# Optimization experiments

Hardware: AMD Instinct MI355X
Metric: run time of the kernel (lower is better)

Reference implementation:

```python
import jax, jax.numpy as jnp
import numpy as np

B = 16384
QD = 2048   # query_dim
KD = 1024   # key_dim
HID = 1024  # hidden_dim = min(QD, KD)
NH = 16     # num_heads
HD = HID // NH  # head_dim = 64
LN_EPS = 1e-5


def _ln(x, w, b):
    m = jnp.mean(x, axis=-1, keepdims=True)
    v = jnp.mean((x - m) ** 2, axis=-1, keepdims=True)
    return (x - m) * jax.lax.rsqrt(v + LN_EPS) * w + b


def _lin(x, W, b):
    return x @ W.T + b


def setup_inputs() -> dict:
    key = jax.random.key(0)
    ks = jax.random.split(key, 12)
    p = lambda k, shape: jax.random.normal(k, shape, jnp.float32) * 0.02
    return dict(
        query_features=jax.random.normal(ks[0], (B, QD), jnp.float32),
        key_features=jax.random.normal(ks[1], (B, KD), jnp.float32),
        Wq=p(ks[2], (HID, QD)), bq=jnp.zeros((HID,), jnp.float32),
        ln_q_w=jnp.ones((HID,), jnp.float32), ln_q_b=jnp.zeros((HID,), jnp.float32),
        Wk=p(ks[3], (HID, KD)), bk=jnp.zeros((HID,), jnp.float32),
        ln_k_w=jnp.ones((HID,), jnp.float32), ln_k_b=jnp.zeros((HID,), jnp.float32),
        Wvq=p(ks[4], (HID, QD)), bvq=jnp.zeros((HID,), jnp.float32),
        Wvk=p(ks[5], (HID, KD)), bvk=jnp.zeros((HID,), jnp.float32),
        Wo=p(ks[6], (QD, HID)), bo=jnp.zeros((QD,), jnp.float32),
        ln_o_w=jnp.ones((QD,), jnp.float32), ln_o_b=jnp.zeros((QD,), jnp.float32),
        Wg1=p(ks[7], (HID, QD + KD)), bg1=jnp.zeros((HID,), jnp.float32),
        Wg2=p(ks[8], (1, HID)), bg2=jnp.zeros((1,), jnp.float32),
        Wc1=p(ks[9], (HID, QD + KD)), bc1=jnp.zeros((HID,), jnp.float32),
        Wc2=p(ks[10], (1, HID)), bc2=jnp.zeros((1,), jnp.float32),
    )


def reference(query_features, key_features,
              Wq, bq, ln_q_w, ln_q_b,
              Wk, bk, ln_k_w, ln_k_b,
              Wvq, bvq, Wvk, bvk,
              Wo, bo, ln_o_w, ln_o_b,
              Wg1, bg1, Wg2, bg2,
              Wc1, bc1, Wc2, bc2):
    b = query_features.shape[0]
    q = _ln(_lin(query_features, Wq, bq), ln_q_w, ln_q_b)      # [B, HID]
    k = _ln(_lin(key_features, Wk, bk), ln_k_w, ln_k_b)        # [B, HID]
    v_q = _lin(query_features, Wvq, bvq)  # computed in torch but unused
    v_k = _lin(key_features, Wvk, bvk)    # [B, HID]
    q = q.reshape(b, NH, HD)
    k = k.reshape(b, NH, HD)
    v_k = v_k.reshape(b, NH, HD)
    # NOTE: attention mixes over the HEAD axis (j == num_heads), per original einsum
    scores = jnp.einsum('bhd,bjd->bhj', q, k) / np.sqrt(HD).astype(np.float32)
    attn = jax.nn.softmax(scores, axis=-1)  # dropout p effectively 0 / eval mode
    attended = jnp.einsum('bhj,bjd->bhd', attn, v_k).reshape(b, HID)
    output = _ln(_lin(attended, Wo, bo), ln_o_w, ln_o_b)       # [B, QD]
    combined = jnp.concatenate([query_features, key_features], axis=1)  # [B, QD+KD]
    gate = jax.nn.sigmoid(_lin(jax.nn.gelu(_lin(combined, Wg1, bg1), approximate=False), Wg2, bg2))
    chem = jax.nn.sigmoid(_lin(jax.nn.gelu(_lin(combined, Wc1, bc1), approximate=False), Wc2, bc2))
    effective_gate = gate * chem  # [B, 1]
    return query_features + effective_gate * output
```

## Files before the change

kernel.cpp:

```cpp
#include <hip/hip_runtime.h>
#include <stdint.h>

#define QD 2048
#define KD 1024
#define HID 1024
#define NH 16
#define HD 64
#define CMBD 3072

typedef float  f32x4   __attribute__((ext_vector_type(4)));
typedef short  short8  __attribute__((ext_vector_type(8)));
typedef short  short4v __attribute__((ext_vector_type(4)));
typedef float  float4v __attribute__((ext_vector_type(4)));

__device__ inline float bf2f(short s) {
  unsigned u = ((unsigned)(unsigned short)s) << 16;
  return __builtin_bit_cast(float, u);
}
__device__ inline short f2bf(float f) {
  unsigned u = __builtin_bit_cast(unsigned, f);
  u = u + 0x7fff + ((u >> 16) & 1);
  return (short)(u >> 16);
}

__global__ void cvt_bf16(const float* __restrict__ s, short* __restrict__ d) {
  size_t i = ((size_t)blockIdx.x * blockDim.x + threadIdx.x) * 4;
  float4v v = *(const float4v*)(s + i);
  short4v o;
  o[0] = f2bf(v[0]); o[1] = f2bf(v[1]); o[2] = f2bf(v[2]); o[3] = f2bf(v[3]);
  *(short4v*)(d + i) = o;
}

__global__ void cvt_concat(const float* __restrict__ s, short* __restrict__ d,
                           int ncols4, int ldd) {
  int i = blockIdx.x * blockDim.x + threadIdx.x;
  int row = i / ncols4;
  int c4  = i - row * ncols4;
  float4v v = *(const float4v*)(s + (size_t)row * (ncols4 * 4) + c4 * 4);
  short4v o;
  o[0] = f2bf(v[0]); o[1] = f2bf(v[1]); o[2] = f2bf(v[2]); o[3] = f2bf(v[3]);
  *(short4v*)(d + (size_t)row * ldd + c4 * 4) = o;
}

#define EPI_NONE 0
#define EPI_GELU 1

typedef const __attribute__((address_space(1))) void gvoid_t;
typedef __attribute__((address_space(3))) void lvoid_t;

#define WAIT_VM(n)  asm volatile("s_waitcnt vmcnt(" #n ")" ::: "memory")

#define APAN(b, kp) (((b) * 2 + (kp)) * 8192)
#define BPAN(b, kp) (32768 + ((b) * 2 + (kp)) * 8192)

#define PHASE_MID                                        \
  __builtin_amdgcn_s_barrier();                          \
  asm volatile("s_waitcnt lgkmcnt(0)" ::: "memory");     \
  __builtin_amdgcn_s_setprio(1);

#define PHASE_END                                        \
  __builtin_amdgcn_s_setprio(0);                         \
  __builtin_amdgcn_s_barrier();

template<int EPI>
__global__ __launch_bounds__(512, 2)
void gemm256(const short* __restrict__ A, size_t lda,
             const short* __restrict__ W,
             const float* __restrict__ bias,
             short* __restrict__ C, int N, int K) {
  extern __shared__ short ls[];
  const int tid  = threadIdx.x;
  const int lane = tid & 63;
  const int wave = tid >> 6;
  const int wm = wave >> 2, wn = wave & 3;
  const int fr = lane & 15, kq4 = lane >> 4;

  const int nwg = gridDim.x * gridDim.y;
  const int lin = blockIdx.y * gridDim.x + blockIdx.x;
  const int cpx = nwg >> 3;
  const int nid = (lin & 7) * cpx + (lin >> 3);
  const int bx = nid % gridDim.x, by = nid / gridDim.x;
  const size_t rowBase = (size_t)by * 256;
  const size_t colBase = (size_t)bx * 256;

  const int NTT = K >> 6;

  f32x4 acc[8][4];
#pragma unroll
  for (int mi = 0; mi < 8; mi++)
#pragma unroll
    for (int ni = 0; ni < 4; ni++) acc[mi][ni] = (f32x4){0.f, 0.f, 0.f, 0.f};

  const int frsw = (kq4 ^ ((fr >> 1) & 3)) * 8;

  const int grow  = tid >> 2;
  const int slotx = (tid & 3) ^ ((tid >> 3) & 3);
  const short* gAlo = A + (rowBase + grow) * lda + slotx * 8;
  const short* gAhi = gAlo + (size_t)128 * lda;
  const short* gBlo = W + (colBase + grow) * (size_t)K + slotx * 8;
  const short* gBhi = gBlo + (size_t)128 * K;
  short* const sdst = ls + tid * 8;

  auto STG_A = [&](int panOff, int kcol) {
    __builtin_amdgcn_global_load_lds((gvoid_t*)(gAlo + kcol), (lvoid_t*)(sdst + panOff),        16, 0, 0);
    __builtin_amdgcn_global_load_lds((gvoid_t*)(gAhi + kcol), (lvoid_t*)(sdst + panOff + 4096), 16, 0, 0);
  };
  auto STG_B = [&](int panOff, int kcol) {
    __builtin_amdgcn_global_load_lds((gvoid_t*)(gBlo + kcol), (lvoid_t*)(sdst + panOff),        16, 0, 0);
    __builtin_amdgcn_global_load_lds((gvoid_t*)(gBhi + kcol), (lvoid_t*)(sdst + panOff + 4096), 16, 0, 0);
  };

  STG_A(APAN(0, 0), 0);  STG_A(APAN(0, 1), 32);
  STG_B(BPAN(0, 0), 0);  STG_B(BPAN(0, 1), 32);
  STG_B(BPAN(1, 0), 64); STG_B(BPAN(1, 1), 96);
  WAIT_VM(4);
  __builtin_amdgcn_s_barrier();

  short8 fa0[8], fa1[8], fb0[4], fb1[4];

  for (int t = 0; t < NTT; t += 2) {
    const bool more = (t + 2 < NTT);
    const int kA1 = (t + 1) * 64;
    const int kE2 = (t + 2) * 64;
    const int kO3 = (t + 3) * 64;

#pragma unroll
    for (int m = 0; m < 4; m++) {
      const int r = (wm * 128 + m * 16 + fr) * 32 + frsw;
      fa0[m * 2 + 0] = *(const short8*)(ls + APAN(0, 0) + r);
      fa0[m * 2 + 1] = *(const short8*)(ls + APAN(0, 1) + r);
    }
#pragma unroll
    for (int n = 0; n < 2; n++) {
      const int r = (wn * 64 + n * 16 + fr) * 32 + frsw;
      fb0[n * 2 + 0] = *(const short8*)(ls + BPAN(0, 0) + r);
      fb0[n * 2 + 1] = *(const short8*)(ls + BPAN(0, 1) + r);
    }
    STG_A(APAN(1, 0), kA1);
    PHASE_MID
#pragma unroll
    for (int m = 0; m < 4; m++)
#pragma unroll
      for (int n = 0; n < 2; n++) {
        acc[m][n] = __builtin_amdgcn_mfma_f32_16x16x32_bf16(fa0[m*2+0], fb0[n*2+0], acc[m][n], 0, 0, 0);
        acc[m][n] = __builtin_amdgcn_mfma_f32_16x16x32_bf16(fa0[m*2+1], fb0[n*2+1], acc[m][n], 0, 0, 0);
      }
    PHASE_END

#pragma unroll
    for (int n = 0; n < 2; n++) {
      const int r = (wn * 64 + (n + 2) * 16 + fr) * 32 + frsw;
      fb1[n * 2 + 0] = *(const short8*)(ls + BPAN(0, 0) + r);
      fb1[n * 2 + 1] = *(const short8*)(ls + BPAN(0, 1) + r);
    }
    STG_A(APAN(1, 1), kA1 + 32);
    PHASE_MID
#pragma unroll
    for (int m = 0; m < 4; m++)
#pragma unroll
      for (int n = 0; n < 2; n++) {
        acc[m][n+2] = __builtin_amdgcn_mfma_f32_16x16x32_bf16(fa0[m*2+0], fb1[n*2+0], acc[m][n+2], 0, 0, 0);
        acc[m][n+2] = __builtin_amdgcn_mfma_f32_16x16x32_bf16(fa0[m*2+1], fb1[n*2+1], acc[m][n+2], 0, 0, 0);
      }
    PHASE_END

#pragma unroll
    for (int m = 0; m < 4; m++) {
      const int r = (wm * 128 + (m + 4) * 16 + fr) * 32 + frsw;
      fa1[m * 2 + 0] = *(const short8*)(ls + APAN(0, 0) + r);
      fa1[m * 2 + 1] = *(const short8*)(ls + APAN(0, 1) + r);
    }
    if (more) STG_B(BPAN(0, 0), kE2);
    PHASE_MID
#pragma unroll
    for (int m = 0; m < 4; m++)
#pragma unroll
      for (int n = 0; n < 2; n++) {
        acc[m+4][n] = __builtin_amdgcn_mfma_f32_16x16x32_bf16(fa1[m*2+0], fb0[n*2+0], acc[m+4][n], 0, 0, 0);
        acc[m+4][n] = __builtin_amdgcn_mfma_f32_16x16x32_bf16(fa1[m*2+1], fb0[n*2+1], acc[m+4][n], 0, 0, 0);
      }
    PHASE_END

    if (more) STG_B(BPAN(0, 1), kE2 + 32);
    PHASE_MID
#pragma unroll
    for (int m = 0; m < 4; m++)
#pragma unroll
      for (int n = 0; n < 2; n++) {
        acc[m+4][n+2] = __builtin_amdgcn_mfma_f32_16x16x32_bf16(fa1[m*2+0], fb1[n*2+0], acc[m+4][n+2], 0, 0, 0);
        acc[m+4][n+2] = __builtin_amdgcn_mfma_f32_16x16x32_bf16(fa1[m*2+1], fb1[n*2+1], acc[m+4][n+2], 0, 0, 0);
      }
    __builtin_amdgcn_s_setprio(0);
    if (more) { WAIT_VM(4); } else { WAIT_VM(0); }
    __builtin_amdgcn_s_barrier();

#pragma unroll
    for (int m = 0; m < 4; m++) {
      const int r = (wm * 128 + m * 16 + fr) * 32 + frsw;
      fa0[m * 2 + 0] = *(const short8*)(ls + APAN(1, 0) + r);
      fa0[m * 2 + 1] = *(const short8*)(ls + APAN(1, 1) + r);
    }
#pragma unroll
    for (int n = 0; n < 2; n++) {
      const int r = (wn * 64 + n * 16 + fr) * 32 + frsw;
      fb0[n * 2 + 0] = *(const short8*)(ls + BPAN(1, 0) + r);
      fb0[n * 2 + 1] = *(const short8*)(ls + BPAN(1, 1) + r);
    }
    if (more) STG_A(APAN(0, 0), kE2);
    PHASE_MID
#pragma unroll
    for (int m = 0; m < 4; m++)
#pragma unroll
      for (int n = 0; n < 2; n++) {
        acc[m][n] = __builtin_amdgcn_mfma_f32_16x16x32_bf16(fa0[m*2+0], fb0[n*2+0], acc[m][n], 0, 0, 0);
        acc[m][n] = __builtin_amdgcn_mfma_f32_16x16x32_bf16(fa0[m*2+1], fb0[n*2+1], acc[m][n], 0, 0, 0);
      }
    PHASE_END

#pragma unroll
    for (int n = 0; n < 2; n++) {
      const int r = (wn * 64 + (n + 2) * 16 + fr) * 32 + frsw;
      fb1[n * 2 + 0] = *(const short8*)(ls + BPAN(1, 0) + r);
      fb1[n * 2 + 1] = *(const short8*)(ls + BPAN(1, 1) + r);
    }
    if (more) STG_A(APAN(0, 1), kE2 + 32);
    PHASE_MID
#pragma unroll
    for (int m = 0; m < 4; m++)
#pragma unroll
      for (int n = 0; n < 2; n++) {
        acc[m][n+2] = __builtin_amdgcn_mfma_f32_16x16x32_bf16(fa0[m*2+0], fb1[n*2+0], acc[m][n+2], 0, 0, 0);
        acc[m][n+2] = __builtin_amdgcn_mfma_f32_16x16x32_bf16(fa0[m*2+1], fb1[n*2+1], acc[m][n+2], 0, 0, 0);
      }
    PHASE_END

#pragma unroll
    for (int m = 0; m < 4; m++) {
      const int r = (wm * 128 + (m + 4) * 16 + fr) * 32 + frsw;
      fa1[m * 2 + 0] = *(const short8*)(ls + APAN(1, 0) + r);
      fa1[m * 2 + 1] = *(const short8*)(ls + APAN(1, 1) + r);
    }
    if (more) STG_B(BPAN(1, 0), kO3);
    PHASE_MID
#pragma unroll
    for (int m = 0; m < 4; m++)
#pragma unroll
      for (int n = 0; n < 2; n++) {
        acc[m+4][n] = __builtin_amdgcn_mfma_f32_16x16x32_bf16(fa1[m*2+0], fb0[n*2+0], acc[m+4][n], 0, 0, 0);
        acc[m+4][n] = __builtin_amdgcn_mfma_f32_16x16x32_bf16(fa1[m*2+1], fb0[n*2+1], acc[m+4][n], 0, 0, 0);
      }
    PHASE_END

    if (more) STG_B(BPAN(1, 1), kO3 + 32);
    PHASE_MID
#pragma unroll
    for (int m = 0; m < 4; m++)
#pragma unroll
      for (int n = 0; n < 2; n++) {
        acc[m+4][n+2] = __builtin_amdgcn_mfma_f32_16x16x32_bf16(fa1[m*2+0], fb1[n*2+0], acc[m+4][n+2], 0, 0, 0);
        acc[m+4][n+2] = __builtin_amdgcn_mfma_f32_16x16x32_bf16(fa1[m*2+1], fb1[n*2+1], acc[m+4][n+2], 0, 0, 0);
      }
    __builtin_amdgcn_s_setprio(0);
    if (more) { WAIT_VM(4); }
    __builtin_amdgcn_s_barrier();
  }

#pragma unroll
  for (int mi = 0; mi < 8; mi++) {
    const size_t row0 = rowBase + wm * 128 + mi * 16 + kq4 * 4;
#pragma unroll
    for (int ni = 0; ni < 4; ni++) {
      const int col = (int)colBase + wn * 64 + ni * 16 + fr;
      const float bv = bias[col];
#pragma unroll
      for (int j = 0; j < 4; j++) {
        float x = acc[mi][ni][j] + bv;
        if (EPI == EPI_GELU) x = 0.5f * x * (1.f + erff(x * 0.70710678118f));
        C[(row0 + j) * (size_t)N + col] = f2bf(x);
      }
    }
  }
}

__device__ inline float2 block_sum2(float a, float b, float* sc) {
#pragma unroll
  for (int o = 32; o >= 1; o >>= 1) {
    a += __shfl_down(a, o);
    b += __shfl_down(b, o);
  }
  const int lane = threadIdx.x & 63, w = threadIdx.x >> 6;
  const int nw = blockDim.x >> 6;
  if (lane == 0) { sc[w * 2] = a; sc[w * 2 + 1] = b; }
  __syncthreads();
  float ra = 0.f, rb = 0.f;
  for (int i = 0; i < nw; i++) { ra += sc[i * 2]; rb += sc[i * 2 + 1]; }
  __syncthreads();
  return make_float2(ra, rb);
}

__global__ __launch_bounds__(256)
void attn_ln(const short* __restrict__ qp, const short* __restrict__ kv,
             const float* __restrict__ lnqw, const float* __restrict__ lnqb,
             const float* __restrict__ lnkw, const float* __restrict__ lnkb,
             short* __restrict__ att) {
  __shared__ float qs[HID];
  __shared__ float ks[NH * 65];
  __shared__ float vs[HID];
  __shared__ float aw[256];
  __shared__ float red[8];
  const int t = threadIdx.x;
  const size_t row = blockIdx.x;

  short4v q4 = *(const short4v*)(qp + row * HID + t * 4);
  short4v k4 = *(const short4v*)(kv + row * 2048 + t * 4);
  short4v v4 = *(const short4v*)(kv + row * 2048 + 1024 + t * 4);
  float qv[4], kvv[4];
  float sq = 0.f, sqq = 0.f, sk = 0.f, skk = 0.f;
#pragma unroll
  for (int i = 0; i < 4; i++) {
    qv[i] = bf2f(q4[i]); sq += qv[i]; sqq += qv[i] * qv[i];
    kvv[i] = bf2f(k4[i]); sk += kvv[i]; skk += kvv[i] * kvv[i];
  }
  float2 rq = block_sum2(sq, sqq, red);
  float mq = rq.x / HID, vq = rq.y / HID - mq * mq;
  float rsq = rsqrtf(vq + 1e-5f);
  float2 rk = block_sum2(sk, skk, red);
  float mk = rk.x / HID, vv = rk.y / HID - mk * mk;
  float rsk = rsqrtf(vv + 1e-5f);
#pragma unroll
  for (int i = 0; i < 4; i++) {
    const int idx = t * 4 + i;
    qs[idx] = (qv[i] - mq) * rsq * lnqw[idx] + lnqb[idx];
    ks[(idx >> 6) * 65 + (idx & 63)] = (kvv[i] - mk) * rsk * lnkw[idx] + lnkb[idx];
    vs[idx] = bf2f(v4[i]);
  }
  __syncthreads();

  const int h = t >> 4, j = t & 15;
  float s = 0.f;
#pragma unroll 8
  for (int d = 0; d < 64; d++) s += qs[h * 64 + d] * ks[j * 65 + d];
  s *= 0.125f;
  float mx = s;
#pragma unroll
  for (int o = 8; o >= 1; o >>= 1) mx = fmaxf(mx, __shfl_xor(mx, o, 16));
  float e = __expf(s - mx);
  float sum = e;
#pragma unroll
  for (int o = 8; o >= 1; o >>= 1) sum += __shfl_xor(sum, o, 16);
  aw[t] = e / sum;
  __syncthreads();

  const int dB = (t & 15) * 4;
  float o0 = 0.f, o1 = 0.f, o2 = 0.f, o3 = 0.f;
#pragma unroll
  for (int jj = 0; jj < 16; jj++) {
    const float w = aw[h * 16 + jj];
    const float* vp = &vs[jj * 64 + dB];
    o0 += w * vp[0]; o1 += w * vp[1]; o2 += w * vp[2]; o3 += w * vp[3];
  }
  short4v o4;
  o4[0] = f2bf(o0); o4[1] = f2bf(o1); o4[2] = f2bf(o2); o4[3] = f2bf(o3);
  *(short4v*)(att + row * HID + h * 64 + dB) = o4;
}

__global__ __launch_bounds__(256)
void gate_kernel(const short* __restrict__ hgc,
                 const float* __restrict__ wg2, const float* __restrict__ bg2,
                 const float* __restrict__ wc2, const float* __restrict__ bc2,
                 float* __restrict__ eg) {
  __shared__ float red[8];
  const int t = threadIdx.x;
  const size_t row = blockIdx.x;
  short4v g4 = *(const short4v*)(hgc + row * 2048 + t * 4);
  short4v c4 = *(const short4v*)(hgc + row * 2048 + 1024 + t * 4);
  float sg = 0.f, sc = 0.f;
#pragma unroll
  for (int i = 0; i < 4; i++) {
    sg += bf2f(g4[i]) * wg2[t * 4 + i];
    sc += bf2f(c4[i]) * wc2[t * 4 + i];
  }
  float2 r = block_sum2(sg, sc, red);
  if (t == 0) {
    float g = 1.f / (1.f + __expf(-(r.x + bg2[0])));
    float c = 1.f / (1.f + __expf(-(r.y + bc2[0])));
    eg[row] = g * c;
  }
}

__global__ __launch_bounds__(256)
void final_kernel(const short* __restrict__ opre, const float* __restrict__ qf,
                  const float* __restrict__ eg,
                  const float* __restrict__ lnow, const float* __restrict__ lnob,
                  float* __restrict__ out) {
  __shared__ float red[8];
  const int t = threadIdx.x;
  const size_t row = blockIdx.x;
  short8 o8 = *(const short8*)(opre + row * QD + t * 8);
  float x[8];
  float s = 0.f, ss = 0.f;
#pragma unroll
  for (int i = 0; i < 8; i++) { x[i] = bf2f(o8[i]); s += x[i]; ss += x[i] * x[i]; }
  float2 r = block_sum2(s, ss, red);
  float m = r.x / QD, v = r.y / QD - m * m;
  float rs = rsqrtf(v + 1e-5f);
  float g = eg[row];
  float4v oa, ob;
#pragma unroll
  for (int i = 0; i < 8; i++) {
    const int c = t * 8 + i;
    float y = (x[i] - m) * rs * lnow[c] + lnob[c];
    float r2 = qf[row * QD + c] + g * y;
    if (i < 4) oa[i] = r2; else ob[i - 4] = r2;
  }
  *(float4v*)(out + row * QD + t * 8) = oa;
  *(float4v*)(out + row * QD + t * 8 + 4) = ob;
}

extern "C" void kernel_launch(void* const* d_in, const int* in_sizes, int n_in,
                              void* d_out, int out_size, void* d_ws, size_t ws_size,
                              hipStream_t stream) {
  const float* qf   = (const float*)d_in[0];
  const float* kf   = (const float*)d_in[1];
  const float* Wq   = (const float*)d_in[2];
  const float* bq   = (const float*)d_in[3];
  const float* lnqw = (const float*)d_in[4];
  const float* lnqb = (const float*)d_in[5];
  const float* Wk   = (const float*)d_in[6];
  const float* bk   = (const float*)d_in[7];
  const float* lnkw = (const float*)d_in[8];
  const float* lnkb = (const float*)d_in[9];
  const float* Wvk  = (const float*)d_in[12];
  const float* bvk  = (const float*)d_in[13];
  const float* Wo   = (const float*)d_in[14];
  const float* bo   = (const float*)d_in[15];
  const float* lnow = (const float*)d_in[16];
  const float* lnob = (const float*)d_in[17];
  const float* Wg1  = (const float*)d_in[18];
  const float* bg1  = (const float*)d_in[19];
  const float* Wg2  = (const float*)d_in[20];
  const float* bg2  = (const float*)d_in[21];
  const float* Wc1  = (const float*)d_in[22];
  const float* bc1  = (const float*)d_in[23];
  const float* Wc2  = (const float*)d_in[24];
  const float* bc2  = (const float*)d_in[25];

  const int rows = in_sizes[0] / QD;

  char* ws = (char*)d_ws;
  size_t off = 0;
  auto alloc = [&](size_t bytes) -> char* {
    char* p = ws + off;
    off += (bytes + 255) & ~(size_t)255;
    return p;
  };
  short* cmb  = (short*)alloc((size_t)rows * CMBD * 2);
  short* wqb  = (short*)alloc((size_t)HID * QD * 2);
  short* wkv  = (short*)alloc((size_t)2 * HID * KD * 2);
  short* wob  = (short*)alloc((size_t)QD * HID * 2);
  short* wgc  = (short*)alloc((size_t)2 * HID * CMBD * 2);
  short* hgc  = (short*)alloc((size_t)rows * 2048 * 2);
  short* qp   = (short*)alloc((size_t)rows * HID * 2);
  short* kvp  = (short*)alloc((size_t)rows * 2048 * 2);
  float* eg   = (float*)alloc((size_t)rows * 4);
  float* bgc  = (float*)alloc(2048 * 4);
  float* bkv  = (float*)alloc(2048 * 4);
  short* att  = hgc;
  short* opre = cmb;

  hipMemcpyAsync(bgc, bg1, HID * 4, hipMemcpyDeviceToDevice, stream);
  hipMemcpyAsync(bgc + HID, bc1, HID * 4, hipMemcpyDeviceToDevice, stream);
  hipMemcpyAsync(bkv, bk, HID * 4, hipMemcpyDeviceToDevice, stream);
  hipMemcpyAsync(bkv + HID, bvk, HID * 4, hipMemcpyDeviceToDevice, stream);

  cvt_concat<<<rows * 2, 256, 0, stream>>>(qf, cmb, QD / 4, CMBD);
  cvt_concat<<<rows, 256, 0, stream>>>(kf, cmb + QD, KD / 4, CMBD);
  cvt_bf16<<<(HID * QD / 4) / 256, 256, 0, stream>>>(Wq, wqb);
  cvt_bf16<<<(HID * KD / 4) / 256, 256, 0, stream>>>(Wk, wkv);
  cvt_bf16<<<(HID * KD / 4) / 256, 256, 0, stream>>>(Wvk, wkv + (size_t)HID * KD);
  cvt_bf16<<<(QD * HID / 4) / 256, 256, 0, stream>>>(Wo, wob);
  cvt_bf16<<<(HID * CMBD / 4) / 256, 256, 0, stream>>>(Wg1, wgc);
  cvt_bf16<<<(HID * CMBD / 4) / 256, 256, 0, stream>>>(Wc1, wgc + (size_t)HID * CMBD);

  hipFuncSetAttribute((const void*)gemm256<EPI_GELU>,
                      hipFuncAttributeMaxDynamicSharedMemorySize, 131072);
  hipFuncSetAttribute((const void*)gemm256<EPI_NONE>,
                      hipFuncAttributeMaxDynamicSharedMemorySize, 131072);

  const dim3 blk(512);
  const int mt = rows / 256;
  const size_t lds = 131072;

  gemm256<EPI_GELU><<<dim3(2048 / 256, mt), blk, lds, stream>>>(cmb, CMBD, wgc, bgc, hgc, 2048, CMBD);
  gate_kernel<<<rows, 256, 0, stream>>>(hgc, Wg2, bg2, Wc2, bc2, eg);
  gemm256<EPI_NONE><<<dim3(1024 / 256, mt), blk, lds, stream>>>(cmb, CMBD, wqb, bq, qp, 1024, QD);
  gemm256<EPI_NONE><<<dim3(2048 / 256, mt), blk, lds, stream>>>(cmb + QD, CMBD, wkv, bkv, kvp, 2048, KD);
  attn_ln<<<rows, 256, 0, stream>>>(qp, kvp, lnqw, lnqb, lnkw, lnkb, att);
  gemm256<EPI_NONE><<<dim3(2048 / 256, mt), blk, lds, stream>>>(att, HID, wob, bo, opre, 2048, HID);
  final_kernel<<<rows, 256, 0, stream>>>(opre, qf, eg, lnow, lnob, (float*)d_out);
}
```

Baseline: 634.4 us.

## Fuse gate/chem second-layer dot products into GEMM epilogue via atomics

The gate GEMM epilogue now applies GELU and immediately dots each row with the second-layer weights. It reduces across lanes and atomically accumulates per-row partial sums into a zeroed buffer, so the bf16 hidden activations are never written and the separate gate kernel is removed. The final kernel applies the sigmoids and combines gate and chem. Separately, the attention LayerNorm merges its two block reductions into one. The cost is float atomics, which add contention and make summation order nondeterministic, plus an extra memset.

```diff
diff --git a/kernel.cpp b/kernel.cpp
--- a/kernel.cpp
+++ b/kernel.cpp
@@ -44,6 +44,7 @@
 
 #define EPI_NONE 0
 #define EPI_GELU 1
+#define EPI_GATE 2
 
 typedef const __attribute__((address_space(1))) void gvoid_t;
 typedef __attribute__((address_space(3))) void lvoid_t;
@@ -67,7 +68,8 @@
 void gemm256(const short* __restrict__ A, size_t lda,
              const short* __restrict__ W,
              const float* __restrict__ bias,
-             short* __restrict__ C, int N, int K) {
+             short* __restrict__ C, int N, int K,
+             const float* __restrict__ w2, float* __restrict__ egp, int rowsTot) {
   extern __shared__ short ls[];
   const int tid  = threadIdx.x;
   const int lane = tid & 63;
@@ -265,35 +267,78 @@
     __builtin_amdgcn_s_barrier();
   }
 
-#pragma unroll
-  for (int mi = 0; mi < 8; mi++) {
-    const size_t row0 = rowBase + wm * 128 + mi * 16 + kq4 * 4;
+  if (EPI == EPI_GATE) {
+    float w2v[4], bvv[4];
 #pragma unroll
     for (int ni = 0; ni < 4; ni++) {
-      const int col = (int)colBase + wn * 64 + ni * 16 + fr;
-      const float bv = bias[col];
+      const int c = (int)colBase + wn * 64 + ni * 16 + fr;
+      w2v[ni] = w2[c]; bvv[ni] = bias[c];
+    }
+    const int half = (colBase >= 1024) ? 1 : 0;
+#pragma unroll
+    for (int mi = 0; mi < 8; mi++) {
+      float sj[4] = {0.f, 0.f, 0.f, 0.f};
+#pragma unroll
+      for (int ni = 0; ni < 4; ni++)
+#pragma unroll
+        for (int j = 0; j < 4; j++) {
+          float x = acc[mi][ni][j] + bvv[ni];
+          float g = 0.5f * x * (1.f + erff(x * 0.70710678118f));
+          sj[j] += g * w2v[ni];
+        }
 #pragma unroll
       for (int j = 0; j < 4; j++) {
-        float x = acc[mi][ni][j] + bv;
-        if (EPI == EPI_GELU) x = 0.5f * x * (1.f + erff(x * 0.70710678118f));
-        C[(row0 + j) * (size_t)N + col] = f2bf(x);
-      }
-    }
-  }
-}
-
-__device__ inline float2 block_sum2(float a, float b, float* sc) {
+#pragma unroll
+        for (int o = 8; o >= 1; o >>= 1) sj[j] += __shfl_xor(sj[j], o);
+        if (fr == 0) {
+          const int row = (int)rowBase + wm * 128 + mi * 16 + kq4 * 4 + j;
+          atomicAdd(egp + half * rowsTot + row, sj[j]);
+        }
+      }
+    }
+  } else {
+#pragma unroll
+    for (int mi = 0; mi < 8; mi++) {
+      const size_t row0 = rowBase + wm * 128 + mi * 16 + kq4 * 4;
+#pragma unroll
+      for (int ni = 0; ni < 4; ni++) {
+        const int col = (int)colBase + wn * 64 + ni * 16 + fr;
+        const float bv = bias[col];
+#pragma unroll
+        for (int j = 0; j < 4; j++) {
+          float x = acc[mi][ni][j] + bv;
+          if (EPI == EPI_GELU) x = 0.5f * x * (1.f + erff(x * 0.70710678118f));
+          C[(row0 + j) * (size_t)N + col] = f2bf(x);
+        }
+      }
+    }
+  }
+}
+
+__device__ inline float4 block_sum4(float a, float b, float c, float d, float* sc) {
 #pragma unroll
   for (int o = 32; o >= 1; o >>= 1) {
-    a += __shfl_down(a, o);
-    b += __shfl_down(b, o);
+    a += __shfl_down(a, o); b += __shfl_down(b, o);
+    c += __shfl_down(c, o); d += __shfl_down(d, o);
   }
   const int lane = threadIdx.x & 63, w = threadIdx.x >> 6;
   const int nw = blockDim.x >> 6;
-  if (lane == 0) { sc[w * 2] = a; sc[w * 2 + 1] = b; }
+  if (lane == 0) { sc[w*4] = a; sc[w*4+1] = b; sc[w*4+2] = c; sc[w*4+3] = d; }
+  __syncthreads();
+  float ra = 0.f, rb = 0.f, rc = 0.f, rd = 0.f;
+  for (int i = 0; i < nw; i++) { ra += sc[i*4]; rb += sc[i*4+1]; rc += sc[i*4+2]; rd += sc[i*4+3]; }
+  __syncthreads();
+  return make_float4(ra, rb, rc, rd);
+}
+__device__ inline float2 block_sum2(float a, float b, float* sc) {
+#pragma unroll
+  for (int o = 32; o >= 1; o >>= 1) { a += __shfl_down(a, o); b += __shfl_down(b, o); }
+  const int lane = threadIdx.x & 63, w = threadIdx.x >> 6;
+  const int nw = blockDim.x >> 6;
+  if (lane == 0) { sc[w*2] = a; sc[w*2+1] = b; }
   __syncthreads();
   float ra = 0.f, rb = 0.f;
-  for (int i = 0; i < nw; i++) { ra += sc[i * 2]; rb += sc[i * 2 + 1]; }
+  for (int i = 0; i < nw; i++) { ra += sc[i*2]; rb += sc[i*2+1]; }
   __syncthreads();
   return make_float2(ra, rb);
 }
@@ -307,7 +352,7 @@
   __shared__ float ks[NH * 65];
   __shared__ float vs[HID];
   __shared__ float aw[256];
-  __shared__ float red[8];
+  __shared__ float red[16];
   const int t = threadIdx.x;
   const size_t row = blockIdx.x;
 
@@ -321,11 +366,10 @@
     qv[i] = bf2f(q4[i]); sq += qv[i]; sqq += qv[i] * qv[i];
     kvv[i] = bf2f(k4[i]); sk += kvv[i]; skk += kvv[i] * kvv[i];
   }
-  float2 rq = block_sum2(sq, sqq, red);
-  float mq = rq.x / HID, vq = rq.y / HID - mq * mq;
+  float4 r4 = block_sum4(sq, sqq, sk, skk, red);
+  float mq = r4.x / HID, vq = r4.y / HID - mq * mq;
   float rsq = rsqrtf(vq + 1e-5f);
-  float2 rk = block_sum2(sk, skk, red);
-  float mk = rk.x / HID, vv = rk.y / HID - mk * mk;
+  float mk = r4.z / HID, vv = r4.w / HID - mk * mk;
   float rsk = rsqrtf(vv + 1e-5f);
 #pragma unroll
   for (int i = 0; i < 4; i++) {
@@ -365,32 +409,9 @@
 }
 
 __global__ __launch_bounds__(256)
-void gate_kernel(const short* __restrict__ hgc,
-                 const float* __restrict__ wg2, const float* __restrict__ bg2,
-                 const float* __restrict__ wc2, const float* __restrict__ bc2,
-                 float* __restrict__ eg) {
-  __shared__ float red[8];
-  const int t = threadIdx.x;
-  const size_t row = blockIdx.x;
-  short4v g4 = *(const short4v*)(hgc + row * 2048 + t * 4);
-  short4v c4 = *(const short4v*)(hgc + row * 2048 + 1024 + t * 4);
-  float sg = 0.f, sc = 0.f;
-#pragma unroll
-  for (int i = 0; i < 4; i++) {
-    sg += bf2f(g4[i]) * wg2[t * 4 + i];
-    sc += bf2f(c4[i]) * wc2[t * 4 + i];
-  }
-  float2 r = block_sum2(sg, sc, red);
-  if (t == 0) {
-    float g = 1.f / (1.f + __expf(-(r.x + bg2[0])));
-    float c = 1.f / (1.f + __expf(-(r.y + bc2[0])));
-    eg[row] = g * c;
-  }
-}
-
-__global__ __launch_bounds__(256)
 void final_kernel(const short* __restrict__ opre, const float* __restrict__ qf,
-                  const float* __restrict__ eg,
+                  const float* __restrict__ egp, int rowsTot,
+                  const float* __restrict__ bg2, const float* __restrict__ bc2,
                   const float* __restrict__ lnow, const float* __restrict__ lnob,
                   float* __restrict__ out) {
   __shared__ float red[8];
@@ -404,7 +425,9 @@
   float2 r = block_sum2(s, ss, red);
   float m = r.x / QD, v = r.y / QD - m * m;
   float rs = rsqrtf(v + 1e-5f);
-  float g = eg[row];
+  float gg = 1.f / (1.f + __expf(-(egp[row] + bg2[0])));
+  float gc = 1.f / (1.f + __expf(-(egp[rowsTot + row] + bc2[0])));
+  float g = gg * gc;
   float4v oa, ob;
 #pragma unroll
   for (int i = 0; i < 8; i++) {
@@ -462,9 +485,10 @@
   short* hgc  = (short*)alloc((size_t)rows * 2048 * 2);
   short* qp   = (short*)alloc((size_t)rows * HID * 2);
   short* kvp  = (short*)alloc((size_t)rows * 2048 * 2);
-  float* eg   = (float*)alloc((size_t)rows * 4);
+  float* egp  = (float*)alloc((size_t)2 * rows * 4);
   float* bgc  = (float*)alloc(2048 * 4);
   float* bkv  = (float*)alloc(2048 * 4);
+  float* w2gc = (float*)alloc(2048 * 4);
   short* att  = hgc;
   short* opre = cmb;
 
@@ -472,6 +496,9 @@
   hipMemcpyAsync(bgc + HID, bc1, HID * 4, hipMemcpyDeviceToDevice, stream);
   hipMemcpyAsync(bkv, bk, HID * 4, hipMemcpyDeviceToDevice, stream);
   hipMemcpyAsync(bkv + HID, bvk, HID * 4, hipMemcpyDeviceToDevice, stream);
+  hipMemcpyAsync(w2gc, Wg2, HID * 4, hipMemcpyDeviceToDevice, stream);
+  hipMemcpyAsync(w2gc + HID, Wc2, HID * 4, hipMemcpyDeviceToDevice, stream);
+  hipMemsetAsync(egp, 0, (size_t)2 * rows * 4, stream);
 
   cvt_concat<<<rows * 2, 256, 0, stream>>>(qf, cmb, QD / 4, CMBD);
   cvt_concat<<<rows, 256, 0, stream>>>(kf, cmb + QD, KD / 4, CMBD);
@@ -482,7 +509,7 @@
   cvt_bf16<<<(HID * CMBD / 4) / 256, 256, 0, stream>>>(Wg1, wgc);
   cvt_bf16<<<(HID * CMBD / 4) / 256, 256, 0, stream>>>(Wc1, wgc + (size_t)HID * CMBD);
 
-  hipFuncSetAttribute((const void*)gemm256<EPI_GELU>,
+  hipFuncSetAttribute((const void*)gemm256<EPI_GATE>,
                       hipFuncAttributeMaxDynamicSharedMemorySize, 131072);
   hipFuncSetAttribute((const void*)gemm256<EPI_NONE>,
                       hipFuncAttributeMaxDynamicSharedMemorySize, 131072);
@@ -491,11 +518,10 @@
   const int mt = rows / 256;
   const size_t lds = 131072;
 
-  gemm256<EPI_GELU><<<dim3(2048 / 256, mt), blk, lds, stream>>>(cmb, CMBD, wgc, bgc, hgc, 2048, CMBD);
-  gate_kernel<<<rows, 256, 0, stream>>>(hgc, Wg2, bg2, Wc2, bc2, eg);
-  gemm256<EPI_NONE><<<dim3(1024 / 256, mt), blk, lds, stream>>>(cmb, CMBD, wqb, bq, qp, 1024, QD);
-  gemm256<EPI_NONE><<<dim3(2048 / 256, mt), blk, lds, stream>>>(cmb + QD, CMBD, wkv, bkv, kvp, 2048, KD);
+  gemm256<EPI_GATE><<<dim3(2048 / 256, mt), blk, lds, stream>>>(cmb, CMBD, wgc, bgc, hgc, 2048, CMBD, w2gc, egp, rows);
+  gemm256<EPI_NONE><<<dim3(1024 / 256, mt), blk, lds, stream>>>(cmb, CMBD, wqb, bq, qp, 1024, QD, nullptr, nullptr, 0);
+  gemm256<EPI_NONE><<<dim3(2048 / 256, mt), blk, lds, stream>>>(cmb + QD, CMBD, wkv, bkv, kvp, 2048, KD, nullptr, nullptr, 0);
   attn_ln<<<rows, 256, 0, stream>>>(qp, kvp, lnqw, lnqb, lnkw, lnkb, att);
-  gemm256<EPI_NONE><<<dim3(2048 / 256, mt), blk, lds, stream>>>(att, HID, wob, bo, opre, 2048, HID);
-  final_kernel<<<rows, 256, 0, stream>>>(opre, qf, eg, lnow, lnob, (float*)d_out);
-}
+  gemm256<EPI_NONE><<<dim3(2048 / 256, mt), blk, lds, stream>>>(att, HID, wob, bo, opre, 2048, HID, nullptr, nullptr, 0);
+  final_kernel<<<rows, 256, 0, stream>>>(opre, qf, egp, rows, bg2, bc2, lnow, lnob, (float*)d_out);
+}
```

Measured after the change: 628.0 us. No clear change (-1.0%).
